# Optimization experiments

Measured on AMD Instinct MI355X. Metric: run time of the kernel, lower is better.

Reference implementation:

```python
import jax, jax.numpy as jnp
import numpy as np

B, C, IC, H, W = 16, 256, 128, 32, 32  # batch, in_channels, inter_channels, spatial
EPS = 1e-5


def _conv1x1(x, w, b=None):
    # x: [B,C,H,W], w: [O,C] -> [B,O,H,W]
    y = jnp.einsum('bchw,oc->bohw', x, w)
    if b is not None:
        y = y + b[None, :, None, None]
    return y


def _dot_kernel(x, wt, wp):
    # relu-matmul attention, symmetrized, degree-rsqrt normalized with zero masking
    b, _, h, w = x.shape
    n = h * w
    t = jnp.maximum(_conv1x1(x, wt), 0.0).reshape(b, -1, n)  # [B,IC,N]
    p = jnp.maximum(_conv1x1(x, wp), 0.0).reshape(b, -1, n)  # [B,IC,N]
    att = jnp.einsum('bcn,bcm->bnm', t, p)                    # [B,N,N]
    att = (att + att.transpose(0, 2, 1)) * 0.5
    d = att.sum(axis=2)                                       # [B,N]
    dinv = jnp.where(d != 0, jax.lax.rsqrt(jnp.where(d != 0, d, 1.0)), 0.0)
    return att * dinv[:, None, :] * dinv[:, :, None]


def _bn(x, gamma, beta):
    # BatchNorm2d in training mode (batch statistics, biased variance)
    mu = jnp.mean(x, axis=(0, 2, 3), keepdims=True)
    var = jnp.mean((x - mu) ** 2, axis=(0, 2, 3), keepdims=True)
    xhat = (x - mu) * jax.lax.rsqrt(var + EPS)
    return xhat * gamma[None, :, None, None] + beta[None, :, None, None]


def setup_inputs() -> dict:
    key = jax.random.key(0)
    ks = jax.random.split(key, 32)
    s = 0.05
    inp = {
        'x':  jax.random.normal(ks[0], (B, C, H, W), jnp.float32),
        'ob': jax.random.normal(ks[1], (B, C, H, W), jnp.float32),
        'od': jax.random.normal(ks[2], (B, C, H, W), jnp.float32),
        'Wt': jax.random.normal(ks[3], (IC, C), jnp.float32) * s,
        'Wp': jax.random.normal(ks[4], (IC, C), jnp.float32) * s,
        'Wgx': jax.random.normal(ks[5], (IC, C), jnp.float32) * s,
        'bgx': jax.random.normal(ks[6], (IC,), jnp.float32) * s,
        'Wgb': jax.random.normal(ks[7], (IC, C), jnp.float32) * s,
        'bgb': jax.random.normal(ks[8], (IC,), jnp.float32) * s,
        'Wgd': jax.random.normal(ks[9], (IC, C), jnp.float32) * s,
        'bgd': jax.random.normal(ks[10], (IC,), jnp.float32) * s,
        'Wwx': jax.random.normal(ks[11], (C, IC), jnp.float32) * s,
        'bwx': jax.random.normal(ks[12], (C,), jnp.float32) * s,
        'Wwb': jax.random.normal(ks[13], (C, IC), jnp.float32) * s,
        'bwb': jax.random.normal(ks[14], (C,), jnp.float32) * s,
        'Wwd': jax.random.normal(ks[15], (C, IC), jnp.float32) * s,
        'bwd': jax.random.normal(ks[16], (C,), jnp.float32) * s,
        'Wwxb': jax.random.normal(ks[17], (C, IC), jnp.float32) * s,
        'bwxb': jax.random.normal(ks[18], (C,), jnp.float32) * s,
        'Wwxd': jax.random.normal(ks[19], (C, IC), jnp.float32) * s,
        'bwxd': jax.random.normal(ks[20], (C,), jnp.float32) * s,
        'gamma1': jnp.ones((C,), jnp.float32),
        'beta1': jnp.zeros((C,), jnp.float32),
        'gamma2': jnp.ones((C,), jnp.float32),
        'beta2': jnp.zeros((C,), jnp.float32),
        'Wout': jax.random.normal(ks[21], (C, C), jnp.float32) * s,
        'bout': jax.random.normal(ks[22], (C,), jnp.float32) * s,
    }
    return inp


def reference(x, ob, od, Wt, Wp, Wgx, bgx, Wgb, bgb, Wgd, bgd,
              Wwx, bwx, Wwb, bwb, Wwd, bwd, Wwxb, bwxb, Wwxd, bwxd,
              gamma1, beta1, gamma2, beta2, Wout, bout):
    b, c, h, w = x.shape
    n = h * w

    def g_tokens(inp, wg, bg):
        return _conv1x1(inp, wg, bg).reshape(b, -1, n).transpose(0, 2, 1)  # [B,N,IC]

    g_x = g_tokens(x, Wgx, bgx)
    g_b = g_tokens(ob, Wgb, bgb)
    g_d = g_tokens(od, Wgd, bgd)

    f_x = _dot_kernel(x, Wt, Wp)
    f_b = _dot_kernel(ob, Wt, Wp)
    f_d = _dot_kernel(od, Wt, Wp)

    def agg(f, g):
        # bmm(f,g).transpose(1,2).view(B,IC,H,W)
        return jnp.einsum('bnm,bmi->bin', f, g).reshape(b, -1, h, w)

    x_self = _conv1x1(agg(f_x, g_x), Wwx, bwx)
    ob_self = _conv1x1(agg(f_b, g_b), Wwb, bwb)
    od_self = _conv1x1(agg(f_d, g_d), Wwd, bwd)
    x_ob_cross = _conv1x1(agg(f_b, g_x), Wwxb, bwxb)
    x_od_cross = _conv1x1(agg(f_d, g_x), Wwxd, bwxd)

    od_final = _bn(od_self + x_ob_cross, gamma1, beta1)
    ob_final = _bn(ob_self + x_od_cross, gamma2, beta2)
    output = _conv1x1(od_final + ob_final + x_self, Wout, bout)
    return output + x
```

## Files before the change

### kernel.cpp

```cpp
#include <hip/hip_runtime.h>

#define GAS __attribute__((address_space(1)))
#define LAS __attribute__((address_space(3)))

typedef __attribute__((ext_vector_type(8))) short short8;
typedef __attribute__((ext_vector_type(4))) float f32x4;
typedef unsigned short u16;

constexpr int cB = 16, cC = 256, cIC = 128, cN = 1024;

__device__ __forceinline__ u16 f2bf(float v) {
    unsigned u = __builtin_bit_cast(unsigned, v);
    return (u16)((u + 0x7fffu + ((u >> 16) & 1u)) >> 16);
}
__device__ __forceinline__ float bf2f(u16 v) {
    unsigned u = ((unsigned)v) << 16;
    return __builtin_bit_cast(float, u);
}
__device__ __forceinline__ float rsz(float d) {
    return (d != 0.0f) ? rsqrtf(d) : 0.0f;
}

template<int N> __device__ __forceinline__ void wait_vmcnt() {
    if constexpr (N == 0) asm volatile("s_waitcnt vmcnt(0)" ::: "memory");
    else if constexpr (N == 1) asm volatile("s_waitcnt vmcnt(1)" ::: "memory");
    else if constexpr (N == 2) asm volatile("s_waitcnt vmcnt(2)" ::: "memory");
    else if constexpr (N == 3) asm volatile("s_waitcnt vmcnt(3)" ::: "memory");
    else if constexpr (N == 4) asm volatile("s_waitcnt vmcnt(4)" ::: "memory");
    else if constexpr (N == 5) asm volatile("s_waitcnt vmcnt(5)" ::: "memory");
    else if constexpr (N == 6) asm volatile("s_waitcnt vmcnt(6)" ::: "memory");
    else if constexpr (N == 8) asm volatile("s_waitcnt vmcnt(8)" ::: "memory");
}

template<int BM, int BN, int WR, int WC, bool BREMAP = false>
__device__ __forceinline__ void gemm_core(
    const u16* __restrict__ Ab, const u16* __restrict__ Ab2, int ksplit, int lda,
    const u16* __restrict__ Bb, int ldb, int K,
    u16* lsA, u16* lsB,
    f32x4 (&acc)[BM/(WR*16)][BN/(WC*16)])
{
    constexpr int THREADS = WR * WC * 64;
    constexpr int MR = BM / (WR * 16), NR = BN / (WC * 16);
    constexpr int ACH = (BM * 64) / (THREADS * 16);
    constexpr int BCH = (BN * 64) / (THREADS * 16);
    constexpr int RPC = THREADS / 4;
    constexpr int ISSUES = ACH + BCH;

    const int tid  = threadIdx.x;
    const int lane = tid & 63;
    const int wave = tid >> 6;
    const int wr = wave / WC, wc = wave % WC;
    const int r0 = tid >> 2, slot = tid & 3;

    auto stage = [&](int buf, int kk) {
        const u16* Ak = (Ab2 != nullptr && kk >= ksplit) ? (Ab2 + (kk - ksplit)) : (Ab + kk);
        const u16* Bk = Bb + (BREMAP ? (((kk >> 7) << 8) + (kk & 127)) : kk);
        #pragma unroll
        for (int c = 0; c < ACH; c++) {
            int row = c * RPC + r0;
            int sk = (slot ^ ((row >> 1) & 3)) << 3;
            __builtin_amdgcn_global_load_lds((GAS void*)(Ak + (size_t)row * lda + sk),
                (LAS void*)(lsA + buf * (BM * 32) + c * (THREADS * 8) + (wave << 9)), 16, 0, 0);
        }
        #pragma unroll
        for (int c = 0; c < BCH; c++) {
            int row = c * RPC + r0;
            int sk = (slot ^ ((row >> 1) & 3)) << 3;
            __builtin_amdgcn_global_load_lds((GAS void*)(Bk + (size_t)row * ldb + sk),
                (LAS void*)(lsB + buf * (BN * 32) + c * (THREADS * 8) + (wave << 9)), 16, 0, 0);
        }
    };

    stage(0, 0);
    const int nt = K >> 5;
    for (int t = 0; t < nt; t++) {
        const int cur = t & 1;
        if (t + 1 < nt) { stage(cur ^ 1, (t + 1) << 5); wait_vmcnt<ISSUES>(); }
        else            wait_vmcnt<0>();
        __builtin_amdgcn_s_barrier();
        asm volatile("" ::: "memory");

        const u16* la = lsA + cur * (BM * 32);
        const u16* lb = lsB + cur * (BN * 32);
        short8 af[MR], bf[NR];
        #pragma unroll
        for (int m = 0; m < MR; m++) {
            int row = wr * (BM / WR) + (m << 4) + (lane & 15);
            af[m] = *(const short8*)&la[(row << 5) + (((lane >> 4) ^ ((row >> 1) & 3)) << 3)];
        }
        #pragma unroll
        for (int n = 0; n < NR; n++) {
            int row = wc * (BN / WC) + (n << 4) + (lane & 15);
            bf[n] = *(const short8*)&lb[(row << 5) + (((lane >> 4) ^ ((row >> 1) & 3)) << 3)];
        }
        #pragma unroll
        for (int m = 0; m < MR; m++)
            #pragma unroll
            for (int n = 0; n < NR; n++)
                acc[m][n] = __builtin_amdgcn_mfma_f32_16x16x32_bf16(af[m], bf[n], acc[m][n], 0, 0, 0);

        asm volatile("s_waitcnt lgkmcnt(0)" ::: "memory");
        __builtin_amdgcn_sched_barrier(0);
        __builtin_amdgcn_s_barrier();
    }
}

template<int BM, int BN, int WR, int WC, bool RELU, bool OBF16, bool RBIAS, bool RESID>
__global__ __launch_bounds__(WR*WC*64) void gemm_bt(
    const u16* __restrict__ A, long long sA, long long sA2, int lda,
    const u16* __restrict__ B, long long sB, long long sB2, int ldb,
    void* __restrict__ C, long long sC, long long sC2, int ldc,
    int K,
    const float* __restrict__ bias, int sb2,
    const float* __restrict__ resid, long long sR)
{
    __shared__ alignas(16) u16 lsA[2 * BM * 32];
    __shared__ alignas(16) u16 lsB[2 * BN * 32];

    const int lane = threadIdx.x & 63;
    const int wave = threadIdx.x >> 6;
    const int wr = wave / WC, wc = wave % WC;
    const int zlo = blockIdx.z & 15, zhi = blockIdx.z >> 4;

    const u16* Ab = A + zlo * sA + zhi * sA2 + (size_t)(blockIdx.x * BM) * lda;
    const u16* Bb = B + zlo * sB + zhi * sB2 + (size_t)(blockIdx.y * BN) * ldb;

    f32x4 acc[BM/(WR*16)][BN/(WC*16)] = {};
    gemm_core<BM, BN, WR, WC>(Ab, nullptr, K, lda, Bb, ldb, K, lsA, lsB, acc);

    const int rowb = blockIdx.x * BM + wr * (BM / WR) + ((lane >> 4) << 2);
    const int colb = blockIdx.y * BN + wc * (BN / WC) + (lane & 15);
    const long long cbase = zlo * sC + zhi * sC2;
    #pragma unroll
    for (int m = 0; m < BM/(WR*16); m++) {
        #pragma unroll
        for (int n = 0; n < BN/(WC*16); n++) {
            #pragma unroll
            for (int r = 0; r < 4; r++) {
                int row = rowb + m * 16 + r;
                int col = colb + n * 16;
                float v = acc[m][n][r];
                if (RBIAS) v += bias[zhi * sb2 + row];
                if (RESID) v += resid[zlo * sR + (size_t)row * ldc + col];
                if (RELU)  v = fmaxf(v, 0.0f);
                if (OBF16) ((u16*)C)[cbase + (size_t)row * ldc + col] = f2bf(v);
                else       ((float*)C)[cbase + (size_t)row * ldc + col] = v;
            }
        }
    }
}

__global__ __launch_bounds__(512) void tp_gemm(
    const u16* __restrict__ XT, const u16* __restrict__ WTP,
    u16* __restrict__ TP, float* __restrict__ CS)
{
    __shared__ alignas(16) u16 lsA[2 * 128 * 32];
    __shared__ alignas(16) u16 lsB[2 * 256 * 32];

    const int nx = blockIdx.x, z = blockIdx.z;
    const u16* Ab = XT + (size_t)z * 262144 + (size_t)(nx * 128) * 256;

    f32x4 acc[4][4] = {};
    gemm_core<128, 256, 2, 4>(Ab, nullptr, 256, 256, WTP, 256, 256, lsA, lsB, acc);

    const int lane = threadIdx.x & 63;
    const int wave = threadIdx.x >> 6;
    const int wr = wave >> 2, wc = wave & 3;
    const int rowb = nx * 128 + wr * 64 + ((lane >> 4) << 2);
    const int colb = wc * 64 + (lane & 15);
    u16* Cb = TP + (size_t)z * 262144;

    float cp[4] = {};
    #pragma unroll
    for (int m = 0; m < 4; m++)
        #pragma unroll
        for (int n = 0; n < 4; n++)
            #pragma unroll
            for (int r = 0; r < 4; r++) {
                float v = fmaxf(acc[m][n][r], 0.0f);
                Cb[(size_t)(rowb + m * 16 + r) * 256 + colb + n * 16] = f2bf(v);
                cp[n] += v;
            }
    #pragma unroll
    for (int n = 0; n < 4; n++) {
        float v = cp[n];
        v += __shfl_xor(v, 16, 64);
        v += __shfl_xor(v, 32, 64);
        if (lane < 16)
            atomicAdd(&CS[z * 256 + colb + n * 16], v);
    }
}

__global__ __launch_bounds__(256) void tpt2(
    const u16* __restrict__ TP, const float* __restrict__ CS,
    u16* __restrict__ TPS, u16* __restrict__ TPSt)
{
    __shared__ u16 ls[64][264];
    __shared__ float ws[256];
    __shared__ float pd[64][4];
    __shared__ float dvs[64];

    const int z = blockIdx.z;
    const int n0 = blockIdx.x << 6;
    const int tid = threadIdx.x;

    ws[tid] = 0.5f * CS[z * 256 + (tid ^ 128)];

    const u16* src = TP + (size_t)z * 262144;
    #pragma unroll
    for (int k = 0; k < 8; k++) {
        int chunk = k * 256 + tid;
        int row = chunk >> 5, c8 = (chunk & 31) << 3;
        *(short8*)&ls[row][c8] = *(const short8*)&src[(size_t)(n0 + row) * 256 + c8];
    }
    __syncthreads();

    {
        const int row = tid >> 2, q = tid & 3;
        float a = 0;
        #pragma unroll 16
        for (int i = 0; i < 64; i++) {
            int c = q * 64 + i;
            a += bf2f(ls[row][c]) * ws[c];
        }
        pd[row][q] = a;
    }
    __syncthreads();
    if (tid < 64) {
        float d = pd[tid][0] + pd[tid][1] + pd[tid][2] + pd[tid][3];
        dvs[tid] = rsz(d);
    }
    __syncthreads();

    u16* So = TPS + (size_t)z * 262144;
    #pragma unroll
    for (int k = 0; k < 8; k++) {
        int chunk = k * 256 + tid;
        int row = chunk >> 5, c8 = (chunk & 31) << 3;
        short8 v = *(const short8*)&ls[row][c8];
        float s = dvs[row];
        short8 o;
        #pragma unroll
        for (int j = 0; j < 8; j++) o[j] = (short)f2bf(bf2f((u16)v[j]) * s);
        *(short8*)&So[(size_t)(n0 + row) * 256 + c8] = o;
    }

    u16* To = TPSt + (size_t)z * 262144 + (size_t)tid * 1024 + n0;
    #pragma unroll
    for (int jb = 0; jb < 8; jb++) {
        short8 o;
        #pragma unroll
        for (int j = 0; j < 8; j++) {
            int n = jb * 8 + j;
            o[j] = (short)f2bf(bf2f(ls[n][tid]) * dvs[n]);
        }
        *(short8*)&To[jb * 8] = o;
    }
}

__global__ __launch_bounds__(256) void g_gemm(
    const u16* __restrict__ XT, const u16* __restrict__ WG,
    const float* __restrict__ BG, u16* __restrict__ G)
{
    __shared__ alignas(16) u16 lsA[2 * 128 * 32];
    __shared__ alignas(16) u16 lsB[2 * 128 * 32];

    const int yb = blockIdx.x, zs = blockIdx.z;
    const int stream = zs >> 4;

    const u16* Ab = WG + stream * 32768;
    const u16* Bb = XT + (size_t)zs * 262144 + (size_t)(yb * 128) * 256;

    f32x4 acc[4][4] = {};
    gemm_core<128, 128, 2, 2>(Ab, nullptr, 256, 256, Bb, 256, 256, lsA, lsB, acc);

    const int lane = threadIdx.x & 63;
    const int wave = threadIdx.x >> 6;
    const int wr = wave >> 1, wc = wave & 1;
    const int rowb = (wr << 6) + ((lane >> 4) << 2);
    const int colb = yb * 128 + (wc << 6) + (lane & 15);
    u16* Gz = G + ((size_t)zs << 17);
    #pragma unroll
    for (int m = 0; m < 4; m++)
        #pragma unroll
        for (int r = 0; r < 4; r++) {
            int row = rowb + m * 16 + r;
            float bias = BG[stream * 128 + row];
            #pragma unroll
            for (int n = 0; n < 4; n++)
                Gz[((size_t)row << 10) + colb + n * 16] = f2bf(acc[m][n][r] + bias);
        }
}

__global__ __launch_bounds__(256) void inner_splitk(
    const u16* __restrict__ TPSt, const u16* __restrict__ G,
    u16* __restrict__ MX, u16* __restrict__ MB, u16* __restrict__ MD)
{
    __shared__ alignas(16) u16 lsA[2 * 128 * 32];
    __shared__ alignas(16) u16 lsB[2 * 128 * 32];

    const int bz = blockIdx.z;
    const int split = bz / 48, z = bz % 48;
    const int which = z >> 4, b = z & 15;
    if (which == 0 && blockIdx.y) return;
    u16* M = (which == 0) ? MX : (which == 1) ? MB : MD;
    const int JD  = (which == 0) ? 128 : 256;
    const int ldc = 2 * JD;
    const int srcz = blockIdx.y ? b : (which * 16 + b);

    const u16* Ab = TPSt + (size_t)z * 262144 + (size_t)(blockIdx.x * 128) * 1024 + split * 512;
    const u16* Bb = G + ((size_t)srcz << 17) + split * 512;

    f32x4 acc[4][4] = {};
    gemm_core<128, 128, 2, 2>(Ab, nullptr, 512, 1024, Bb, 1024, 512, lsA, lsB, acc);

    const int lane = threadIdx.x & 63;
    const int wave = threadIdx.x >> 6;
    const int wr = wave >> 1, wc = wave & 1;
    const int rowb = blockIdx.x * 128 + (wr << 6) + ((lane >> 4) << 2);
    const int colb = blockIdx.y * 128 + (wc << 6) + (lane & 15);
    u16* Cb = M + (size_t)b * (256 * ldc);
    #pragma unroll
    for (int m = 0; m < 4; m++)
        #pragma unroll
        for (int n = 0; n < 4; n++)
            #pragma unroll
            for (int r = 0; r < 4; r++) {
                int row = (rowb + m * 16 + r) ^ 128;
                int col = split * JD + colb + n * 16;
                Cb[(size_t)row * ldc + col] = f2bf(acc[m][n][r]);
            }
}

__global__ __launch_bounds__(512) void fold_gemm(
    const u16* __restrict__ WF2, const u16* __restrict__ MX,
    const u16* __restrict__ MB, const u16* __restrict__ MD,
    u16* __restrict__ FF2)
{
    __shared__ alignas(16) u16 lsA[2 * 128 * 32];
    __shared__ alignas(16) u16 lsB[2 * 256 * 32];

    const int z = blockIdx.z, q = z >> 4, b = z & 15;
    const int pr = (q == 4) ? 2 : (q >> 1);
    const int side = (q == 1 || q == 3) ? 1 : 0;

    const u16* Ab = WF2 + q * 65536 + (size_t)(blockIdx.x * 128) * 256;

    f32x4 acc[4][4] = {};
    if (q == 4) {
        const u16* Bb = MX + (size_t)b * 65536;
        gemm_core<128, 256, 2, 4, false>(Ab, nullptr, 256, 256, Bb, 256, 256, lsA, lsB, acc);
    } else {
        const u16* Mp = (q == 1 || q == 2) ? MB : MD;
        const int coff = side ? 128 : 0;
        const u16* Bb = Mp + (size_t)b * 131072 + coff;
        gemm_core<128, 256, 2, 4, true>(Ab, nullptr, 256, 256, Bb, 512, 256, lsA, lsB, acc);
    }

    const int lane = threadIdx.x & 63;
    const int wave = threadIdx.x >> 6;
    const int wr = wave >> 2, wc = wave & 3;
    const int rowb = blockIdx.x * 128 + wr * 64 + ((lane >> 4) << 2);
    const int colb = wc * 64 + (lane & 15);
    u16* Cb = FF2 + (size_t)pr * 2097152 + (size_t)b * 131072;
    #pragma unroll
    for (int m = 0; m < 4; m++)
        #pragma unroll
        for (int n = 0; n < 4; n++)
            #pragma unroll
            for (int r = 0; r < 4; r++)
                Cb[(size_t)(rowb + m * 16 + r) * 512 + side * 256 + colb + n * 16]
                    = f2bf(acc[m][n][r]);
}

__global__ __launch_bounds__(512) void outer_gemm(
    const u16* __restrict__ TPS, const u16* __restrict__ FF2,
    u16* __restrict__ SALL, float* __restrict__ BNA)
{
    __shared__ alignas(16) u16 lsA[2 * 128 * 32];
    __shared__ alignas(16) u16 lsB[2 * 256 * 32];

    const int z = blockIdx.z, zhi = z >> 4, b = z & 15;
    const int sa1[3] = {2, 1, 0}, sa2[3] = {1, 2, 0};
    const int K = (zhi == 2) ? 256 : 512;

    const u16* A1 = TPS + (size_t)(sa1[zhi] * 16 + b) * 262144 + (size_t)(blockIdx.x * 128) * 256;
    const u16* A2 = (zhi == 2) ? nullptr
                  : TPS + (size_t)(sa2[zhi] * 16 + b) * 262144 + (size_t)(blockIdx.x * 128) * 256;
    const u16* Bb = FF2 + (size_t)zhi * 2097152 + (size_t)b * 131072;

    f32x4 acc[4][4] = {};
    gemm_core<128, 256, 2, 4>(A1, A2, 256, 256, Bb, 512, K, lsA, lsB, acc);

    const int lane = threadIdx.x & 63;
    const int wave = threadIdx.x >> 6;
    const int wr = wave >> 2, wc = wave & 3;
    const int rowb = blockIdx.x * 128 + wr * 64 + ((lane >> 4) << 2);
    const int colb = wc * 64 + (lane & 15);

    u16* Cb = SALL + (size_t)b * 786432;
    float csum[4] = {}, csq[4] = {};
    #pragma unroll
    for (int m = 0; m < 4; m++)
        #pragma unroll
        for (int n = 0; n < 4; n++)
            #pragma unroll
            for (int r = 0; r < 4; r++) {
                float v = acc[m][n][r];
                Cb[(size_t)(rowb + m * 16 + r) * 768 + zhi * 256 + colb + n * 16] = f2bf(v);
                csum[n] += v;
                csq[n] += v * v;
            }
    if (zhi < 2) {
        #pragma unroll
        for (int n = 0; n < 4; n++) {
            float s = csum[n], q = csq[n];
            s += __shfl_xor(s, 16, 64); s += __shfl_xor(s, 32, 64);
            q += __shfl_xor(q, 16, 64); q += __shfl_xor(q, 32, 64);
            if (lane < 16) {
                atomicAdd(&BNA[zhi * 512 + colb + n * 16], s);
                atomicAdd(&BNA[zhi * 512 + 256 + colb + n * 16], q);
            }
        }
    }
}

__global__ __launch_bounds__(256) void bnscale(
    const float* __restrict__ Wout, const float* __restrict__ g1, const float* __restrict__ be1,
    const float* __restrict__ g2, const float* __restrict__ be2,
    const float* __restrict__ bwx, const float* __restrict__ bout,
    const float* __restrict__ BNA, u16* __restrict__ WoutS, float* __restrict__ BIAS2)
{
    int o = blockIdx.x, c = threadIdx.x;
    const float inv = 1.0f / 16384.0f;
    float m1 = BNA[c] * inv;
    float v1 = BNA[256 + c] * inv - m1 * m1;
    float sc1 = g1[c] * rsqrtf(v1 + 1e-5f), sh1 = be1[c] - m1 * sc1;
    float m2 = BNA[512 + c] * inv;
    float v2 = BNA[768 + c] * inv - m2 * m2;
    float sc2 = g2[c] * rsqrtf(v2 + 1e-5f), sh2 = be2[c] - m2 * sc2;
    float wv = Wout[o * 256 + c];
    WoutS[o * 768 + c]       = f2bf(wv * sc1);
    WoutS[o * 768 + 256 + c] = f2bf(wv * sc2);
    WoutS[o * 768 + 512 + c] = f2bf(wv);
    __shared__ float red[256];
    red[c] = wv * (sh1 + sh2 + bwx[c]);
    __syncthreads();
    for (int s = 128; s; s >>= 1) { if (c < s) red[c] += red[c + s]; __syncthreads(); }
    if (c == 0) BIAS2[o] = red[0] + bout[o];
}

__global__ __launch_bounds__(256) void prep_transpose(
    const float* __restrict__ x, const float* __restrict__ ob,
    const float* __restrict__ od, u16* __restrict__ xt,
    const float* Wt, const float* Wp,
    const float* Wgx, const float* Wgb, const float* Wgd,
    const float* bgx, const float* bgb, const float* bgd,
    const float* Wwd, const float* Wwxb, const float* Wwb,
    const float* Wwxd, const float* Wwx,
    u16* wtp, u16* wg, u16* wf2, float* bg,
    float* __restrict__ ZZ)
{
    const int tid = threadIdx.x;
    if (blockIdx.z == 48) {
        int base = (blockIdx.y * 16 + blockIdx.x) * 1024;
        #pragma unroll
        for (int l = 0; l < 4; l++) {
            int t = base + l * 256 + tid;
            wtp[t] = f2bf(t < 32768 ? Wt[t] : Wp[t - 32768]);
            if (t < 32768) {
                wg[t] = f2bf(Wgx[t]); wg[32768 + t] = f2bf(Wgb[t]); wg[65536 + t] = f2bf(Wgd[t]);
            }
            {
                int o = t >> 8, k = t & 255, j = k & 127;
                const float* Wq[5] = {Wwd, Wwxb, Wwb, Wwxd, Wwx};
                #pragma unroll
                for (int q = 0; q < 5; q++)
                    wf2[q * 65536 + t] = f2bf(0.5f * Wq[q][o * 128 + j]);
            }
            if (t < 384) bg[t] = (t < 128) ? bgx[t] : (t < 256) ? bgb[t - 128] : bgd[t - 256];
            if (t < 13312) ZZ[t] = 0.0f;
        }
        return;
    }
    __shared__ float ls[64][68];
    const int z = blockIdx.z, which = z >> 4, b = z & 15;
    const float* src = (which == 0) ? x : (which == 1) ? ob : od;
    const float* s = src + (size_t)b * cC * cN;
    u16* dst = xt + (size_t)z * (cN * cC);
    const int n0 = blockIdx.x << 6, c0 = blockIdx.y << 6;

    const int cl0 = tid >> 4, n4 = (tid & 15) << 2;
    #pragma unroll
    for (int p = 0; p < 4; p++) {
        int cl = cl0 + (p << 4);
        f32x4 v = *(const f32x4*)&s[(size_t)(c0 + cl) * cN + n0 + n4];
        ls[cl][n4] = v[0]; ls[cl][n4 + 1] = v[1]; ls[cl][n4 + 2] = v[2]; ls[cl][n4 + 3] = v[3];
    }
    __syncthreads();
    const int nl0 = tid >> 3, c8 = (tid & 7) << 3;
    #pragma unroll
    for (int q = 0; q < 2; q++) {
        int nl = nl0 + (q << 5);
        short8 o;
        #pragma unroll
        for (int j = 0; j < 8; j++) o[j] = (short)f2bf(ls[c8 + j][nl]);
        *(short8*)&dst[(size_t)(n0 + nl) * 256 + c0 + c8] = o;
    }
}

extern "C" void kernel_launch(void* const* d_in, const int* in_sizes, int n_in,
                              void* d_out, int out_size, void* d_ws, size_t ws_size,
                              hipStream_t stream)
{
    const float* x    = (const float*)d_in[0];
    const float* ob   = (const float*)d_in[1];
    const float* od   = (const float*)d_in[2];
    const float* Wt   = (const float*)d_in[3];
    const float* Wp   = (const float*)d_in[4];
    const float* Wgx  = (const float*)d_in[5];
    const float* bgx  = (const float*)d_in[6];
    const float* Wgb  = (const float*)d_in[7];
    const float* bgb  = (const float*)d_in[8];
    const float* Wgd  = (const float*)d_in[9];
    const float* bgd  = (const float*)d_in[10];
    const float* Wwx  = (const float*)d_in[11];
    const float* bwx  = (const float*)d_in[12];
    const float* Wwb  = (const float*)d_in[13];
    const float* Wwd  = (const float*)d_in[15];
    const float* Wwxb = (const float*)d_in[17];
    const float* Wwxd = (const float*)d_in[19];
    const float* g1   = (const float*)d_in[21];
    const float* be1  = (const float*)d_in[22];
    const float* g2   = (const float*)d_in[23];
    const float* be2  = (const float*)d_in[24];
    const float* Wout = (const float*)d_in[25];
    const float* bout = (const float*)d_in[26];
    float* out = (float*)d_out;

    char* w = (char*)d_ws;
    u16*   XT    = (u16*)(w);
    u16*   TP    = (u16*)(w + 25165824);
    u16*   TPS   = (u16*)(w + 50331648);
    u16*   TPSt  = (u16*)(w + 75497472);
    u16*   G     = (u16*)(w + 100663296);
    u16*   MX    = (u16*)(w + 113246208);
    u16*   MB    = (u16*)(w + 115343360);
    u16*   MD    = (u16*)(w + 119537664);
    u16*   FF2   = (u16*)(w + 123731968);
    u16*   WTP   = (u16*)(w + 136314880);
    u16*   WG    = (u16*)(w + 136445952);
    u16*   WF2   = (u16*)(w + 136642560);
    u16*   WoutS = (u16*)(w + 137297920);
    float* BGf   = (float*)(w + 137691136);
    float* BIAS2 = (float*)(w + 137693184);
    float* ZZ    = (float*)(w + 137697280);

    float* CS   = ZZ;
    float* BNA  = ZZ + 12288;
    u16*   SALL = TP;

    prep_transpose<<<dim3(16, 4, 49), 256, 0, stream>>>(
        x, ob, od, XT, Wt, Wp, Wgx, Wgb, Wgd, bgx, bgb, bgd,
        Wwd, Wwxb, Wwb, Wwxd, Wwx, WTP, WG, WF2, BGf, ZZ);

    tp_gemm<<<dim3(8, 1, 48), 512, 0, stream>>>(XT, WTP, TP, CS);

    tpt2<<<dim3(16, 1, 48), 256, 0, stream>>>(TP, CS, TPS, TPSt);

    g_gemm<<<dim3(8, 1, 48), 256, 0, stream>>>(XT, WG, BGf, G);

    inner_splitk<<<dim3(2, 2, 96), 256, 0, stream>>>(TPSt, G, MX, MB, MD);

    fold_gemm<<<dim3(2, 1, 80), 512, 0, stream>>>(WF2, MX, MB, MD, FF2);

    outer_gemm<<<dim3(8, 1, 48), 512, 0, stream>>>(TPS, FF2, SALL, BNA);

    bnscale<<<dim3(256), 256, 0, stream>>>(Wout, g1, be1, g2, be2, bwx, bout,
                                           BNA, WoutS, BIAS2);

    gemm_bt<128, 128, 2, 2, false, false, true, true><<<dim3(2, 8, 16), 256, 0, stream>>>(
        WoutS, 0, 0, 768,  SALL, 786432, 0, 768,  out, 262144, 0, 1024,
        768, BIAS2, 0, x, 262144);
}
```

Before: 142.2 us.

## Triple-buffer GEMM core LDS staging and merge tp/g GEMMs into one launch

The shared GEMM core now uses a three-stage LDS ring buffer, prefetching two K-tiles ahead instead of one so global-to-LDS loads overlap more with MFMA work. All kernels using the core get triple-sized LDS buffers. Separately, the t/p projection GEMM and the g-token GEMM are fused into one launch of 576 blocks, with g now using 128x256 tiles on 512 threads. This removes a kernel launch and fills the device better, at the cost of more LDS per block, which may lower occupancy.

```diff
diff --git a/kernel.cpp b/kernel.cpp
--- a/kernel.cpp
+++ b/kernel.cpp
@@ -71,12 +71,15 @@
         }
     };
 
+    const int nt = K >> 5;
     stage(0, 0);
-    const int nt = K >> 5;
+    if (nt > 1) stage(1, 32);
+
+    int cur = 0;
     for (int t = 0; t < nt; t++) {
-        const int cur = t & 1;
-        if (t + 1 < nt) { stage(cur ^ 1, (t + 1) << 5); wait_vmcnt<ISSUES>(); }
-        else            wait_vmcnt<0>();
+        if (t + 2 < nt) { stage((cur + 2 >= 3) ? cur - 1 : cur + 2, (t + 2) << 5); wait_vmcnt<2 * ISSUES>(); }
+        else if (t + 1 < nt) wait_vmcnt<ISSUES>();
+        else                 wait_vmcnt<0>();
         __builtin_amdgcn_s_barrier();
         asm volatile("" ::: "memory");
 
@@ -102,6 +105,7 @@
         asm volatile("s_waitcnt lgkmcnt(0)" ::: "memory");
         __builtin_amdgcn_sched_barrier(0);
         __builtin_amdgcn_s_barrier();
+        cur = (cur + 1 >= 3) ? 0 : cur + 1;
     }
 }
 
@@ -114,8 +118,8 @@
     const float* __restrict__ bias, int sb2,
     const float* __restrict__ resid, long long sR)
 {
-    __shared__ alignas(16) u16 lsA[2 * BM * 32];
-    __shared__ alignas(16) u16 lsB[2 * BN * 32];
+    __shared__ alignas(16) u16 lsA[3 * BM * 32];
+    __shared__ alignas(16) u16 lsB[3 * BN * 32];
 
     const int lane = threadIdx.x & 63;
     const int wave = threadIdx.x >> 6;
@@ -150,44 +154,73 @@
     }
 }
 
-__global__ __launch_bounds__(512) void tp_gemm(
+__global__ __launch_bounds__(512) void tpg_gemm(
     const u16* __restrict__ XT, const u16* __restrict__ WTP,
-    u16* __restrict__ TP, float* __restrict__ CS)
-{
-    __shared__ alignas(16) u16 lsA[2 * 128 * 32];
-    __shared__ alignas(16) u16 lsB[2 * 256 * 32];
-
-    const int nx = blockIdx.x, z = blockIdx.z;
-    const u16* Ab = XT + (size_t)z * 262144 + (size_t)(nx * 128) * 256;
-
-    f32x4 acc[4][4] = {};
-    gemm_core<128, 256, 2, 4>(Ab, nullptr, 256, 256, WTP, 256, 256, lsA, lsB, acc);
-
+    const u16* __restrict__ WG, const float* __restrict__ BG,
+    u16* __restrict__ TP, float* __restrict__ CS, u16* __restrict__ G)
+{
+    __shared__ alignas(16) u16 lsA[3 * 128 * 32];
+    __shared__ alignas(16) u16 lsB[3 * 256 * 32];
+
+    const int id = blockIdx.x;
     const int lane = threadIdx.x & 63;
     const int wave = threadIdx.x >> 6;
     const int wr = wave >> 2, wc = wave & 3;
-    const int rowb = nx * 128 + wr * 64 + ((lane >> 4) << 2);
-    const int colb = wc * 64 + (lane & 15);
-    u16* Cb = TP + (size_t)z * 262144;
-
-    float cp[4] = {};
-    #pragma unroll
-    for (int m = 0; m < 4; m++)
-        #pragma unroll
-        for (int n = 0; n < 4; n++)
+
+    if (id < 384) {
+        const int nx = id & 7, z = id >> 3;
+        const u16* Ab = XT + (size_t)z * 262144 + (size_t)(nx * 128) * 256;
+
+        f32x4 acc[4][4] = {};
+        gemm_core<128, 256, 2, 4>(Ab, nullptr, 256, 256, WTP, 256, 256, lsA, lsB, acc);
+
+        const int rowb = nx * 128 + wr * 64 + ((lane >> 4) << 2);
+        const int colb = wc * 64 + (lane & 15);
+        u16* Cb = TP + (size_t)z * 262144;
+
+        float cp[4] = {};
+        #pragma unroll
+        for (int m = 0; m < 4; m++)
+            #pragma unroll
+            for (int n = 0; n < 4; n++)
+                #pragma unroll
+                for (int r = 0; r < 4; r++) {
+                    float v = fmaxf(acc[m][n][r], 0.0f);
+                    Cb[(size_t)(rowb + m * 16 + r) * 256 + colb + n * 16] = f2bf(v);
+                    cp[n] += v;
+                }
+        #pragma unroll
+        for (int n = 0; n < 4; n++) {
+            float v = cp[n];
+            v += __shfl_xor(v, 16, 64);
+            v += __shfl_xor(v, 32, 64);
+            if (lane < 16)
+                atomicAdd(&CS[z * 256 + colb + n * 16], v);
+        }
+    } else {
+        const int gi = id - 384;
+        const int yb = gi & 3, zs = gi >> 2;
+        const int stream = zs >> 4;
+
+        const u16* Ab = WG + stream * 32768;
+        const u16* Bb = XT + (size_t)zs * 262144 + (size_t)(yb * 256) * 256;
+
+        f32x4 acc[4][4] = {};
+        gemm_core<128, 256, 2, 4>(Ab, nullptr, 256, 256, Bb, 256, 256, lsA, lsB, acc);
+
+        const int rowb = wr * 64 + ((lane >> 4) << 2);
+        const int colb = yb * 256 + wc * 64 + (lane & 15);
+        u16* Gz = G + ((size_t)zs << 17);
+        #pragma unroll
+        for (int m = 0; m < 4; m++)
             #pragma unroll
             for (int r = 0; r < 4; r++) {
-                float v = fmaxf(acc[m][n][r], 0.0f);
-                Cb[(size_t)(rowb + m * 16 + r) * 256 + colb + n * 16] = f2bf(v);
-                cp[n] += v;
-            }
-    #pragma unroll
-    for (int n = 0; n < 4; n++) {
-        float v = cp[n];
-        v += __shfl_xor(v, 16, 64);
-        v += __shfl_xor(v, 32, 64);
-        if (lane < 16)
-            atomicAdd(&CS[z * 256 + colb + n * 16], v);
+                int row = rowb + m * 16 + r;
+                float bias = BG[stream * 128 + row];
+                #pragma unroll
+                for (int n = 0; n < 4; n++)
+                    Gz[((size_t)row << 10) + colb + n * 16] = f2bf(acc[m][n][r] + bias);
+            }
     }
 }
 
@@ -258,46 +291,12 @@
     }
 }
 
-__global__ __launch_bounds__(256) void g_gemm(
-    const u16* __restrict__ XT, const u16* __restrict__ WG,
-    const float* __restrict__ BG, u16* __restrict__ G)
-{
-    __shared__ alignas(16) u16 lsA[2 * 128 * 32];
-    __shared__ alignas(16) u16 lsB[2 * 128 * 32];
-
-    const int yb = blockIdx.x, zs = blockIdx.z;
-    const int stream = zs >> 4;
-
-    const u16* Ab = WG + stream * 32768;
-    const u16* Bb = XT + (size_t)zs * 262144 + (size_t)(yb * 128) * 256;
-
-    f32x4 acc[4][4] = {};
-    gemm_core<128, 128, 2, 2>(Ab, nullptr, 256, 256, Bb, 256, 256, lsA, lsB, acc);
-
-    const int lane = threadIdx.x & 63;
-    const int wave = threadIdx.x >> 6;
-    const int wr = wave >> 1, wc = wave & 1;
-    const int rowb = (wr << 6) + ((lane >> 4) << 2);
-    const int colb = yb * 128 + (wc << 6) + (lane & 15);
-    u16* Gz = G + ((size_t)zs << 17);
-    #pragma unroll
-    for (int m = 0; m < 4; m++)
-        #pragma unroll
-        for (int r = 0; r < 4; r++) {
-            int row = rowb + m * 16 + r;
-            float bias = BG[stream * 128 + row];
-            #pragma unroll
-            for (int n = 0; n < 4; n++)
-                Gz[((size_t)row << 10) + colb + n * 16] = f2bf(acc[m][n][r] + bias);
-        }
-}
-
 __global__ __launch_bounds__(256) void inner_splitk(
     const u16* __restrict__ TPSt, const u16* __restrict__ G,
     u16* __restrict__ MX, u16* __restrict__ MB, u16* __restrict__ MD)
 {
-    __shared__ alignas(16) u16 lsA[2 * 128 * 32];
-    __shared__ alignas(16) u16 lsB[2 * 128 * 32];
+    __shared__ alignas(16) u16 lsA[3 * 128 * 32];
+    __shared__ alignas(16) u16 lsB[3 * 128 * 32];
 
     const int bz = blockIdx.z;
     const int split = bz / 48, z = bz % 48;
@@ -337,8 +336,8 @@
     const u16* __restrict__ MB, const u16* __restrict__ MD,
     u16* __restrict__ FF2)
 {
-    __shared__ alignas(16) u16 lsA[2 * 128 * 32];
-    __shared__ alignas(16) u16 lsB[2 * 256 * 32];
+    __shared__ alignas(16) u16 lsA[3 * 128 * 32];
+    __shared__ alignas(16) u16 lsB[3 * 256 * 32];
 
     const int z = blockIdx.z, q = z >> 4, b = z & 15;
     const int pr = (q == 4) ? 2 : (q >> 1);
@@ -377,8 +376,8 @@
     const u16* __restrict__ TPS, const u16* __restrict__ FF2,
     u16* __restrict__ SALL, float* __restrict__ BNA)
 {
-    __shared__ alignas(16) u16 lsA[2 * 128 * 32];
-    __shared__ alignas(16) u16 lsB[2 * 256 * 32];
+    __shared__ alignas(16) u16 lsA[3 * 128 * 32];
+    __shared__ alignas(16) u16 lsB[3 * 256 * 32];
 
     const int z = blockIdx.z, zhi = z >> 4, b = z & 15;
     const int sa1[3] = {2, 1, 0}, sa2[3] = {1, 2, 0};
@@ -564,11 +563,9 @@
         x, ob, od, XT, Wt, Wp, Wgx, Wgb, Wgd, bgx, bgb, bgd,
         Wwd, Wwxb, Wwb, Wwxd, Wwx, WTP, WG, WF2, BGf, ZZ);
 
-    tp_gemm<<<dim3(8, 1, 48), 512, 0, stream>>>(XT, WTP, TP, CS);
+    tpg_gemm<<<dim3(576), 512, 0, stream>>>(XT, WTP, WG, BGf, TP, CS, G);
 
     tpt2<<<dim3(16, 1, 48), 256, 0, stream>>>(TP, CS, TPS, TPSt);
-
-    g_gemm<<<dim3(8, 1, 48), 256, 0, stream>>>(XT, WG, BGf, G);
 
     inner_splitk<<<dim3(2, 2, 96), 256, 0, stream>>>(TPSt, G, MX, MB, MD);
 
```

New measurement: 148.0 us. +4.1%, slower.
